# Kernel optimization log

Hardware: AMD Instinct MI355X
Metric: run time of the kernel (lower is better)

Reference implementation:

```python
import jax, jax.numpy as jnp
import numpy as np

NUM_CLASSES = 1000
N, C = 8192, 256

def setup_inputs() -> dict:
    key = jax.random.key(0)
    k1, k2, k3 = jax.random.split(key, 3)
    p = jax.random.normal(k1, (N, C), dtype=jnp.float32)
    z = jax.random.normal(k2, (N, C), dtype=jnp.float32)
    t = jax.random.uniform(k3, (N, NUM_CLASSES), dtype=jnp.float32, minval=1e-4, maxval=1.0)
    targets = t / jnp.sum(t, axis=1, keepdims=True)  # valid soft-label distribution
    return {"p": p, "z": z, "targets": targets}

def reference(p, z, targets):
    z = jax.lax.stop_gradient(z)  # z.detach()
    # F.normalize(dim=1), eps=1e-12
    p = p / jnp.maximum(jnp.linalg.norm(p, axis=1, keepdims=True), 1e-12)
    zn = z / jnp.maximum(jnp.linalg.norm(z, axis=1, keepdims=True), 1e-12)
    dot_product = -jnp.matmul(p, zn.T)  # [N, N]
    # entropy of soft targets, NaN rows (any exact-zero entry) zeroed
    prod = targets * jnp.log(targets)
    entr = -jnp.sum(prod, axis=1)
    entr = jnp.where(jnp.isnan(entr), 0.0, entr)
    norm_entr = entr / jnp.log(jnp.float32(NUM_CLASSES))
    r = 1.0 - norm_entr
    mask1 = jnp.outer(r, r)  # [N, N]
    # cosine similarity Gram of targets (torch cosine_similarity eps=1e-8)
    tnorm = jnp.linalg.norm(targets, axis=1)
    denom = jnp.maximum(tnorm[:, None] * tnorm[None, :], 1e-8)
    mask2 = jnp.matmul(targets, targets.T) / denom  # [N, N]
    n = dot_product.shape[0]
    mask_anchor_out = 1.0 - jnp.eye(n, dtype=dot_product.dtype)
    mask_combined = mask1 * mask2 * mask_anchor_out
    sel = dot_product * mask_combined
    # mean over nonzero entries (jit-safe: sum / count of nonzeros)
    nz = (sel != 0.0)
    return jnp.sum(sel) / jnp.sum(nz).astype(sel.dtype)
```

## Files before the change

### kernel.cpp

```cpp
#include <hip/hip_runtime.h>
#include <math.h>

#define NROWS 8192
#define CDIM 256
#define KDIM 1000
#define KPAD 1024

#define BC 128
#define BK 64
#define BI 8

typedef __attribute__((ext_vector_type(8))) short bf16x8;
typedef __attribute__((ext_vector_type(4))) float f32x4;
typedef _Float16 f16;
typedef __attribute__((ext_vector_type(4))) _Float16 f16x4;

__device__ __forceinline__ unsigned short f2bf(float x) {
  unsigned int u = __float_as_uint(x);
  u += 0x7fffu + ((u >> 16) & 1u);
  return (unsigned short)(u >> 16);
}
__device__ __forceinline__ float bf2f(unsigned short h) {
  return __uint_as_float(((unsigned int)h) << 16);
}

__device__ __forceinline__ void gl16(const void* g, void* l) {
  __builtin_amdgcn_global_load_lds(
      (const __attribute__((address_space(1))) unsigned int*)g,
      (__attribute__((address_space(3))) unsigned int*)l, 16, 0, 0);
}

__global__ __launch_bounds__(256, 4) void prep_kernel(
    const float* __restrict__ p, const float* __restrict__ z,
    const float* __restrict__ t,
    unsigned short* __restrict__ gAhi, unsigned short* __restrict__ gAlo,
    unsigned short* __restrict__ gBhi, unsigned short* __restrict__ gBlo,
    unsigned short* __restrict__ gUhi, unsigned short* __restrict__ gUlo,
    float* __restrict__ diag) {
  __shared__ float tbuf[8 * 1028];
  __shared__ float st_s[8], uu_s[8], sa_s[8], sb_s[8];
  __shared__ double r_s[8];
  const int tid = threadIdx.x;
  const int w = tid >> 6, lane = tid & 63;
  const int stripe = blockIdx.x;
  const int istep = stripe >> 2;
  const int qtr = stripe & 3;
  const int i0 = stripe * 8;

#pragma unroll
  for (int rr = 0; rr < 2; ++rr) {
    const int row = 2 * w + rr;
    const float* trow = t + (size_t)(i0 + row) * KDIM;
    float stt = 0.f, ent = 0.f, zfl = 0.f;
#pragma unroll
    for (int c = 0; c < 4; ++c) {
      const int k4 = c * 64 + lane;
      float4 v = make_float4(0.f, 0.f, 0.f, 0.f);
      if (k4 < 250) {
        v = *(const float4*)(trow + k4 * 4);
        const float vv[4] = {v.x, v.y, v.z, v.w};
#pragma unroll
        for (int q = 0; q < 4; ++q) {
          stt += vv[q] * vv[q];
          if (vv[q] > 0.f) ent += vv[q] * logf(vv[q]);
          else zfl = 1.f;
        }
      }
      *(float4*)&tbuf[row * 1028 + k4 * 4] = v;
    }
#pragma unroll
    for (int off = 32; off; off >>= 1) {
      stt += __shfl_xor(stt, off);
      ent += __shfl_xor(ent, off);
      zfl += __shfl_xor(zfl, off);
    }
    if (lane == 0) {
      const float tnorm = sqrtf(stt);
      st_s[row] = 1.f / tnorm;
      uu_s[row] = stt / (tnorm * tnorm);
      const float entr = (zfl > 0.f) ? 0.f : (-ent);
      r_s[row] = 1.0 - (double)entr / log(1000.0);
    }
  }
  __syncthreads();

#pragma unroll
  for (int it = 0; it < 4; ++it) {
    const int item = it * 256 + tid;
    const int kt = item >> 7;
    const int kf = (item >> 4) & 7;
    const int cl = item & 15;
    const int kcl = kf * 16 + cl;
    unsigned int hi[4], lo[4];
#pragma unroll
    for (int q = 0; q < 4; ++q) {
      const int r0 = 2 * q, r1 = r0 + 1;
      const float v0 = tbuf[r0 * 1028 + kt * 128 + kcl] * st_s[r0];
      const float v1 = tbuf[r1 * 1028 + kt * 128 + kcl] * st_s[r1];
      const unsigned short h0 = f2bf(v0), h1 = f2bf(v1);
      hi[q] = (unsigned int)h0 | ((unsigned int)h1 << 16);
      const unsigned short e0 = f2bf(v0 - bf2f(h0));
      const unsigned short e1 = f2bf(v1 - bf2f(h1));
      lo[q] = (unsigned int)e0 | ((unsigned int)e1 << 16);
    }
    const size_t off = ((size_t)(kt * 256 + istep)) * 8192
                       + (size_t)kf * 1024 + (size_t)(qtr * 16 + cl) * 16;
    *(uint4*)((char*)gUhi + off) = make_uint4(hi[0], hi[1], hi[2], hi[3]);
    *(uint4*)((char*)gUlo + off) = make_uint4(lo[0], lo[1], lo[2], lo[3]);
  }
  __syncthreads();

  float* ptile = tbuf;
  float* ztile = tbuf + 8 * 260;
#pragma unroll
  for (int rr = 0; rr < 2; ++rr) {
    const int row = 2 * w + rr;
    const float* prow = p + (size_t)(i0 + row) * CDIM;
    const float* zrow = z + (size_t)(i0 + row) * CDIM;
    const float4 pv = *(const float4*)(prow + lane * 4);
    const float4 zv = *(const float4*)(zrow + lane * 4);
    *(float4*)&ptile[row * 260 + lane * 4] = pv;
    *(float4*)&ztile[row * 260 + lane * 4] = zv;
    float sp = pv.x * pv.x + pv.y * pv.y + pv.z * pv.z + pv.w * pv.w;
    float sz = zv.x * zv.x + zv.y * zv.y + zv.z * zv.z + zv.w * zv.w;
    float spz = pv.x * zv.x + pv.y * zv.y + pv.z * zv.z + pv.w * zv.w;
#pragma unroll
    for (int off = 32; off; off >>= 1) {
      sp += __shfl_xor(sp, off);
      sz += __shfl_xor(sz, off);
      spz += __shfl_xor(spz, off);
    }
    if (lane == 0) {
      const double r = r_s[row];
      const float pnorm = sqrtf(sp), znorm = sqrtf(sz);
      const float sav = (float)(r / fmax((double)pnorm, 1e-12));
      const float sbv = (float)(r / fmax((double)znorm, 1e-12));
      sa_s[row] = sav; sb_s[row] = sbv;
      diag[i0 + row] = spz * sav * sbv * uu_s[row];
    }
  }
  __syncthreads();

  {
    const int cfg = tid >> 4;
    const int cl = tid & 15;
    const int crd = cfg * 16 + cl;
#pragma unroll 1
    for (int which = 0; which < 2; ++which) {
      const float* tile = which ? ztile : ptile;
      const float* ss = which ? sb_s : sa_s;
      unsigned short* ghi = which ? gBhi : gAhi;
      unsigned short* glo = which ? gBlo : gAlo;
      unsigned int hi[4], lo[4];
#pragma unroll
      for (int q = 0; q < 4; ++q) {
        const int r0 = 2 * q, r1 = r0 + 1;
        const float v0 = tile[r0 * 260 + crd] * ss[r0];
        const float v1 = tile[r1 * 260 + crd] * ss[r1];
        const unsigned short h0 = f2bf(v0), h1 = f2bf(v1);
        hi[q] = (unsigned int)h0 | ((unsigned int)h1 << 16);
        const unsigned short e0 = f2bf(v0 - bf2f(h0));
        const unsigned short e1 = f2bf(v1 - bf2f(h1));
        lo[q] = (unsigned int)e0 | ((unsigned int)e1 << 16);
      }
      const size_t off = ((size_t)((cfg >> 3) * 256 + istep)) * 8192
                         + (size_t)(cfg & 7) * 1024 + (size_t)(qtr * 16 + cl) * 16;
      *(uint4*)((char*)ghi + off) = make_uint4(hi[0], hi[1], hi[2], hi[3]);
      *(uint4*)((char*)glo + off) = make_uint4(lo[0], lo[1], lo[2], lo[3]);
    }
  }
}

__global__ __launch_bounds__(512, 2) void mfma_gemm_kernel(
    const unsigned short* __restrict__ gAhi, const unsigned short* __restrict__ gAlo,
    const unsigned short* __restrict__ gBhi, const unsigned short* __restrict__ gBlo,
    const unsigned short* __restrict__ gUhi, const unsigned short* __restrict__ gUlo,
    f16* __restrict__ part1, f16* __restrict__ part2, int steps) {
  __shared__ unsigned short lds[3][6][4096];
  const int tid = threadIdx.x;
  const int lane = tid & 63;
  const int wid = tid >> 6;
  const int wr = wid >> 1, wc = wid & 1;
  const int ct = blockIdx.x, kt = blockIdx.y, zc = blockIdx.z;
  const int istep0 = zc * steps;

  f32x4 acc1[2][4], acc2[2][4];
#pragma unroll
  for (int c = 0; c < 2; ++c)
#pragma unroll
    for (int k = 0; k < 4; ++k) {
      acc1[c][k] = (f32x4){0.f, 0.f, 0.f, 0.f};
      acc2[c][k] = (f32x4){0.f, 0.f, 0.f, 0.f};
    }

  const char* sA0 = (const char*)gAhi;
  const char* sA1 = (const char*)gAlo;
  const char* sB0 = (const char*)gBhi;
  const char* sB1 = (const char*)gBlo;
  const char* sU0 = (const char*)gUhi;
  const char* sU1 = (const char*)gUlo;

  auto stage = [&](int buf, int s) {
    const size_t ab = ((size_t)(ct * 256 + istep0 + s)) * 8192 + (size_t)tid * 16;
    const size_t ub = ((size_t)(kt * 256 + istep0 + s)) * 8192 + (size_t)tid * 16;
    gl16(sA0 + ab, &lds[buf][0][tid * 8]);
    gl16(sA1 + ab, &lds[buf][1][tid * 8]);
    gl16(sB0 + ab, &lds[buf][2][tid * 8]);
    gl16(sB1 + ab, &lds[buf][3][tid * 8]);
    gl16(sU0 + ub, &lds[buf][4][tid * 8]);
    gl16(sU1 + ub, &lds[buf][5][tid * 8]);
  };

  stage(0, 0);
  if (steps > 1) stage(1, 1);
  for (int s = 0; s < steps; ++s) {
    const int cur = s % 3;
    if (s < steps - 1) {
      asm volatile("s_waitcnt vmcnt(6)" ::: "memory");
    } else {
      asm volatile("s_waitcnt vmcnt(0)" ::: "memory");
    }
    __builtin_amdgcn_s_barrier();
    asm volatile("" ::: "memory");
    if (s + 2 < steps) stage((s + 2) % 3, s + 2);

    bf16x8 ah[2], al[2], bh[2], bl[2], uh[4], ul[4];
#pragma unroll
    for (int c = 0; c < 2; ++c) {
      const int cf = wr * 2 + c;
      ah[c] = *(const bf16x8*)&lds[cur][0][(cf * 64 + lane) * 8];
      al[c] = *(const bf16x8*)&lds[cur][1][(cf * 64 + lane) * 8];
      bh[c] = *(const bf16x8*)&lds[cur][2][(cf * 64 + lane) * 8];
      bl[c] = *(const bf16x8*)&lds[cur][3][(cf * 64 + lane) * 8];
    }
#pragma unroll
    for (int k = 0; k < 4; ++k) {
      const int kf = wc * 4 + k;
      uh[k] = *(const bf16x8*)&lds[cur][4][(kf * 64 + lane) * 8];
      ul[k] = *(const bf16x8*)&lds[cur][5][(kf * 64 + lane) * 8];
    }
    __builtin_amdgcn_s_setprio(1);
#pragma unroll
    for (int k = 0; k < 4; ++k)
#pragma unroll
      for (int c = 0; c < 2; ++c) {
        acc1[c][k] = __builtin_amdgcn_mfma_f32_16x16x32_bf16(ah[c], uh[k], acc1[c][k], 0, 0, 0);
        acc1[c][k] = __builtin_amdgcn_mfma_f32_16x16x32_bf16(al[c], uh[k], acc1[c][k], 0, 0, 0);
        acc1[c][k] = __builtin_amdgcn_mfma_f32_16x16x32_bf16(ah[c], ul[k], acc1[c][k], 0, 0, 0);
        acc2[c][k] = __builtin_amdgcn_mfma_f32_16x16x32_bf16(bh[c], uh[k], acc2[c][k], 0, 0, 0);
        acc2[c][k] = __builtin_amdgcn_mfma_f32_16x16x32_bf16(bl[c], uh[k], acc2[c][k], 0, 0, 0);
        acc2[c][k] = __builtin_amdgcn_mfma_f32_16x16x32_bf16(bh[c], ul[k], acc2[c][k], 0, 0, 0);
      }
    __builtin_amdgcn_s_setprio(0);
  }

  f16* o1 = part1 + (size_t)zc * (CDIM * KPAD);
  f16* o2 = part2 + (size_t)zc * (CDIM * KPAD);
#pragma unroll
  for (int c = 0; c < 2; ++c)
#pragma unroll
    for (int k = 0; k < 4; ++k)
#pragma unroll
      for (int j = 0; j < 4; ++j) {
        const int cg = ct * 128 + (wr * 2 + c) * 16 + (lane >> 4) * 4 + j;
        const int kg = kt * 128 + (wc * 4 + k) * 16 + (lane & 15);
        o1[(size_t)cg * KPAD + kg] = (f16)acc1[c][k][j];
        o2[(size_t)cg * KPAD + kg] = (f16)acc2[c][k][j];
      }
}

__global__ __launch_bounds__(256) void reduce_h_kernel(
    const f16* __restrict__ part1, const f16* __restrict__ part2,
    double* __restrict__ bsum, int split) {
  const int tid = threadIdx.x;
  const size_t base = ((size_t)blockIdx.x * 256 + tid) * 4;
  double m1[4] = {0, 0, 0, 0}, m2[4] = {0, 0, 0, 0};
#pragma unroll 4
  for (int zz = 0; zz < split; ++zz) {
    const f16x4 a = *(const f16x4*)(part1 + (size_t)zz * (CDIM * KPAD) + base);
    const f16x4 b = *(const f16x4*)(part2 + (size_t)zz * (CDIM * KPAD) + base);
#pragma unroll
    for (int e = 0; e < 4; ++e) {
      m1[e] += (double)(float)a[e];
      m2[e] += (double)(float)b[e];
    }
  }
  double s = 0.0;
#pragma unroll
  for (int e = 0; e < 4; ++e) s += m1[e] * m2[e];
  __shared__ double red[256];
  red[tid] = s;
  __syncthreads();
  for (int off = 128; off; off >>= 1) {
    if (tid < off) red[tid] += red[tid + off];
    __syncthreads();
  }
  if (tid == 0) bsum[blockIdx.x] = red[0];
}

__global__ __launch_bounds__(256) void rowstats_kernel(
    const float* __restrict__ p, const float* __restrict__ z,
    const float* __restrict__ t,
    float* __restrict__ sa, float* __restrict__ sb,
    float* __restrict__ st, float* __restrict__ diag) {
  const int i = blockIdx.x;
  const int tid = threadIdx.x;
  const float pv = p[(size_t)i * CDIM + tid];
  const float zv = z[(size_t)i * CDIM + tid];
  float sp = pv * pv, sz = zv * zv, spz = pv * zv;
  float stt = 0.f, ent = 0.f, zfl = 0.f;
  const float* trow = t + (size_t)i * KDIM;
  for (int k = tid; k < KDIM; k += 256) {
    const float tv = trow[k];
    stt += tv * tv;
    if (tv > 0.f) ent += tv * logf(tv);
    else zfl = 1.f;
  }
#pragma unroll
  for (int off = 32; off; off >>= 1) {
    sp  += __shfl_down(sp, off);
    sz  += __shfl_down(sz, off);
    spz += __shfl_down(spz, off);
    stt += __shfl_down(stt, off);
    ent += __shfl_down(ent, off);
    zfl += __shfl_down(zfl, off);
  }
  __shared__ float wred[4][6];
  const int wid = tid >> 6, lane = tid & 63;
  if (lane == 0) {
    wred[wid][0] = sp;  wred[wid][1] = sz;  wred[wid][2] = spz;
    wred[wid][3] = stt; wred[wid][4] = ent; wred[wid][5] = zfl;
  }
  __syncthreads();
  if (tid == 0) {
    sp  = wred[0][0] + wred[1][0] + wred[2][0] + wred[3][0];
    sz  = wred[0][1] + wred[1][1] + wred[2][1] + wred[3][1];
    spz = wred[0][2] + wred[1][2] + wred[2][2] + wred[3][2];
    stt = wred[0][3] + wred[1][3] + wred[2][3] + wred[3][3];
    ent = wred[0][4] + wred[1][4] + wred[2][4] + wred[3][4];
    zfl = wred[0][5] + wred[1][5] + wred[2][5] + wred[3][5];
    const float pnorm = sqrtf(sp);
    const float znorm = sqrtf(sz);
    const float tnorm = sqrtf(stt);
    const float entr = (zfl > 0.f) ? 0.f : (-ent);
    const double r = 1.0 - (double)entr / log(1000.0);
    const float sav = (float)(r / fmax((double)pnorm, 1e-12));
    const float sbv = (float)(r / fmax((double)znorm, 1e-12));
    const float stv = 1.f / tnorm;
    const float uu = stt / (tnorm * tnorm);
    sa[i] = sav; sb[i] = sbv; st[i] = stv;
    diag[i] = spz * sav * sbv * uu;
  }
}

__global__ __launch_bounds__(256) void fp32_gemm_kernel(
    const float* __restrict__ p, const float* __restrict__ z,
    const float* __restrict__ t,
    const float* __restrict__ sa, const float* __restrict__ sb,
    const float* __restrict__ st,
    float* __restrict__ part1, float* __restrict__ part2, int ichunk) {
  __shared__ float As[BI][BC];
  __shared__ float Bs[BI][BC];
  __shared__ float Us[BI][BK];
  const int tid = threadIdx.x;
  const int c0 = blockIdx.x * BC;
  const int k0 = blockIdx.y * BK;
  const int i0 = blockIdx.z * ichunk;
  float acc1[8][4] = {{0.f}};
  float acc2[8][4] = {{0.f}};
  const int tc = tid & 15;
  const int tk = tid >> 4;
  const int lrow = tid >> 5;
  const int lcolA = (tid & 31) * 4;
  const int lcolU = (tid & 31) * 2;
  for (int ib = 0; ib < ichunk; ib += BI) {
    const int i = i0 + ib + lrow;
    const float sav = sa[i], sbv = sb[i], stv = st[i];
    const float4 pv = *(const float4*)(p + (size_t)i * CDIM + c0 + lcolA);
    const float4 zv = *(const float4*)(z + (size_t)i * CDIM + c0 + lcolA);
    const int kk = k0 + lcolU;
    const float u0 = (kk     < KDIM) ? t[(size_t)i * KDIM + kk]     * stv : 0.f;
    const float u1 = (kk + 1 < KDIM) ? t[(size_t)i * KDIM + kk + 1] * stv : 0.f;
    __syncthreads();
    *(float4*)&As[lrow][lcolA] = make_float4(pv.x * sav, pv.y * sav, pv.z * sav, pv.w * sav);
    *(float4*)&Bs[lrow][lcolA] = make_float4(zv.x * sbv, zv.y * sbv, zv.z * sbv, zv.w * sbv);
    Us[lrow][lcolU] = u0;
    Us[lrow][lcolU + 1] = u1;
    __syncthreads();
#pragma unroll
    for (int ii = 0; ii < BI; ++ii) {
      const float4 a0 = *(const float4*)&As[ii][tc * 8];
      const float4 a1 = *(const float4*)&As[ii][tc * 8 + 4];
      const float4 b0 = *(const float4*)&Bs[ii][tc * 8];
      const float4 b1 = *(const float4*)&Bs[ii][tc * 8 + 4];
      const float4 u  = *(const float4*)&Us[ii][tk * 4];
      const float a[8] = {a0.x, a0.y, a0.z, a0.w, a1.x, a1.y, a1.z, a1.w};
      const float b[8] = {b0.x, b0.y, b0.z, b0.w, b1.x, b1.y, b1.z, b1.w};
      const float uv[4] = {u.x, u.y, u.z, u.w};
#pragma unroll
      for (int m = 0; m < 8; ++m)
#pragma unroll
        for (int n = 0; n < 4; ++n) {
          acc1[m][n] = fmaf(a[m], uv[n], acc1[m][n]);
          acc2[m][n] = fmaf(b[m], uv[n], acc2[m][n]);
        }
    }
  }
  float* o1 = part1 + (size_t)blockIdx.z * (CDIM * KPAD);
  float* o2 = part2 + (size_t)blockIdx.z * (CDIM * KPAD);
#pragma unroll
  for (int m = 0; m < 8; ++m) {
    const int c = c0 + tc * 8 + m;
    const int k = k0 + tk * 4;
    *(float4*)&o1[(size_t)c * KPAD + k] = *(const float4*)acc1[m];
    *(float4*)&o2[(size_t)c * KPAD + k] = *(const float4*)acc2[m];
  }
}

__global__ __launch_bounds__(256) void reduce_kernel(
    const float* __restrict__ part1, const float* __restrict__ part2,
    double* __restrict__ bsum, int split) {
  const int tid = threadIdx.x;
  double s = 0.0;
  for (int r = 0; r < 4; ++r) {
    const size_t idx = (size_t)blockIdx.x * 1024 + (size_t)r * 256 + tid;
    double m1 = 0.0, m2 = 0.0;
    for (int zz = 0; zz < split; ++zz) {
      m1 += (double)part1[(size_t)zz * (CDIM * KPAD) + idx];
      m2 += (double)part2[(size_t)zz * (CDIM * KPAD) + idx];
    }
    s += m1 * m2;
  }
  __shared__ double red[256];
  red[tid] = s;
  __syncthreads();
  for (int off = 128; off; off >>= 1) {
    if (tid < off) red[tid] += red[tid + off];
    __syncthreads();
  }
  if (tid == 0) bsum[blockIdx.x] = red[0];
}

__global__ __launch_bounds__(256) void final_kernel(
    const double* __restrict__ bsum, const float* __restrict__ diag,
    float* __restrict__ out, int nb) {
  const int tid = threadIdx.x;
  double s = 0.0;
  for (int i = tid; i < nb; i += 256) s += bsum[i];
  double d = 0.0;
  for (int i = tid; i < NROWS; i += 256) d += (double)diag[i];
  __shared__ double red[256];
  red[tid] = s;
  __syncthreads();
  for (int off = 128; off; off >>= 1) {
    if (tid < off) red[tid] += red[tid + off];
    __syncthreads();
  }
  double s_all = red[0];
  __syncthreads();
  red[tid] = d;
  __syncthreads();
  for (int off = 128; off; off >>= 1) {
    if (tid < off) red[tid] += red[tid + off];
    __syncthreads();
  }
  if (tid == 0) {
    const double s_diag = red[0];
    const double sel_sum = -(s_all - s_diag);
    const double cnt = (double)NROWS * (double)NROWS - (double)NROWS;
    out[0] = (float)(sel_sum / cnt);
  }
}

extern "C" void kernel_launch(void* const* d_in, const int* in_sizes, int n_in,
                              void* d_out, int out_size, void* d_ws, size_t ws_size,
                              hipStream_t stream) {
  const float* p = (const float*)d_in[0];
  const float* z = (const float*)d_in[1];
  const float* t = (const float*)d_in[2];
  float* out = (float*)d_out;
  char* ws = (char*)d_ws;

  float* sa = (float*)ws;
  float* sb = sa + NROWS;
  float* st = sb + NROWS;
  float* diag = st + NROWS;
  const size_t statsB = (size_t)4 * NROWS * sizeof(float);

  const size_t planeA = (size_t)2 * 256 * 8 * 1024;
  const size_t planeU = (size_t)8 * 256 * 8 * 1024;
  const size_t chunkH = (size_t)CDIM * KPAD * 2;
  const size_t chunkF = (size_t)CDIM * KPAD * 4;

  int split = 16;
  while (split > 4 &&
         statsB + 4 * planeA + 2 * planeU + (size_t)split * 2 * chunkH + 8192 > ws_size)
    split >>= 1;
  const bool use_mfma =
      statsB + 4 * planeA + 2 * planeU + (size_t)split * 2 * chunkH + 8192 <= ws_size;

  if (use_mfma) {
    char* base = ws + statsB;
    unsigned short* gAhi = (unsigned short*)(base);
    unsigned short* gAlo = (unsigned short*)(base + planeA);
    unsigned short* gBhi = (unsigned short*)(base + 2 * planeA);
    unsigned short* gBlo = (unsigned short*)(base + 3 * planeA);
    unsigned short* gUhi = (unsigned short*)(base + 4 * planeA);
    unsigned short* gUlo = (unsigned short*)(base + 4 * planeA + planeU);
    f16* part1 = (f16*)(base + 4 * planeA + 2 * planeU);
    f16* part2 = part1 + (size_t)split * (CDIM * KPAD);
    double* bsum = (double*)(part2 + (size_t)split * (CDIM * KPAD));
    const int steps = (NROWS / split) / 32;

    hipLaunchKernelGGL(prep_kernel, dim3(1024), dim3(256), 0, stream,
                       p, z, t, gAhi, gAlo, gBhi, gBlo, gUhi, gUlo, diag);
    hipLaunchKernelGGL(mfma_gemm_kernel, dim3(2, 8, split), dim3(512), 0, stream,
                       gAhi, gAlo, gBhi, gBlo, gUhi, gUlo, part1, part2, steps);
    hipLaunchKernelGGL(reduce_h_kernel, dim3(256), dim3(256), 0, stream,
                       part1, part2, bsum, split);
    hipLaunchKernelGGL(final_kernel, dim3(1), dim3(256), 0, stream,
                       bsum, diag, out, 256);
  } else {
    int osplit = 16;
    while (osplit > 1 &&
           statsB + (size_t)osplit * chunkF * 2 + 8192 > ws_size)
      osplit >>= 1;
    float* part1 = (float*)(ws + statsB);
    float* part2 = part1 + (size_t)osplit * (CDIM * KPAD);
    double* bsum = (double*)(part2 + (size_t)osplit * (CDIM * KPAD));
    hipLaunchKernelGGL(rowstats_kernel, dim3(NROWS), dim3(256), 0, stream,
                       p, z, t, sa, sb, st, diag);
    hipLaunchKernelGGL(fp32_gemm_kernel, dim3(CDIM / BC, KPAD / BK, osplit),
                       dim3(256), 0, stream,
                       p, z, t, sa, sb, st, part1, part2, NROWS / osplit);
    hipLaunchKernelGGL(reduce_kernel, dim3(256), dim3(256), 0, stream,
                       part1, part2, bsum, osplit);
    hipLaunchKernelGGL(final_kernel, dim3(1), dim3(256), 0, stream,
                       bsum, diag, out, 256);
  }
}
```

Measured before the change: 65.34 us.

## Halve GEMM block to 4 waves with larger per-wave C tile

Shrinks the MFMA GEMM block from 512 to 256 threads. Each wave now covers 4 C-fragments instead of 2, so each U fragment loaded from LDS feeds more MFMAs, and U is loaded in two halves to limit register pressure. Each thread issues twice as many global-to-LDS copies per stage, with the vmcnt wait adjusted to match. This cuts LDS read traffic per MFMA but raises VGPR use (64 accumulators) and halves the waves per block, which may reduce latency hiding.

```diff
diff --git a/kernel.cpp b/kernel.cpp
--- a/kernel.cpp
+++ b/kernel.cpp
@@ -171,7 +171,7 @@
   }
 }
 
-__global__ __launch_bounds__(512, 2) void mfma_gemm_kernel(
+__global__ __launch_bounds__(256, 1) void mfma_gemm_kernel(
     const unsigned short* __restrict__ gAhi, const unsigned short* __restrict__ gAlo,
     const unsigned short* __restrict__ gBhi, const unsigned short* __restrict__ gBlo,
     const unsigned short* __restrict__ gUhi, const unsigned short* __restrict__ gUlo,
@@ -184,31 +184,32 @@
   const int ct = blockIdx.x, kt = blockIdx.y, zc = blockIdx.z;
   const int istep0 = zc * steps;
 
-  f32x4 acc1[2][4], acc2[2][4];
-#pragma unroll
-  for (int c = 0; c < 2; ++c)
+  f32x4 acc1[4][4], acc2[4][4];
+#pragma unroll
+  for (int c = 0; c < 4; ++c)
 #pragma unroll
     for (int k = 0; k < 4; ++k) {
       acc1[c][k] = (f32x4){0.f, 0.f, 0.f, 0.f};
       acc2[c][k] = (f32x4){0.f, 0.f, 0.f, 0.f};
     }
 
-  const char* sA0 = (const char*)gAhi;
-  const char* sA1 = (const char*)gAlo;
-  const char* sB0 = (const char*)gBhi;
-  const char* sB1 = (const char*)gBlo;
-  const char* sU0 = (const char*)gUhi;
-  const char* sU1 = (const char*)gUlo;
+  const char* sP[6] = {(const char*)gAhi, (const char*)gAlo,
+                       (const char*)gBhi, (const char*)gBlo,
+                       (const char*)gUhi, (const char*)gUlo};
 
   auto stage = [&](int buf, int s) {
     const size_t ab = ((size_t)(ct * 256 + istep0 + s)) * 8192 + (size_t)tid * 16;
     const size_t ub = ((size_t)(kt * 256 + istep0 + s)) * 8192 + (size_t)tid * 16;
-    gl16(sA0 + ab, &lds[buf][0][tid * 8]);
-    gl16(sA1 + ab, &lds[buf][1][tid * 8]);
-    gl16(sB0 + ab, &lds[buf][2][tid * 8]);
-    gl16(sB1 + ab, &lds[buf][3][tid * 8]);
-    gl16(sU0 + ub, &lds[buf][4][tid * 8]);
-    gl16(sU1 + ub, &lds[buf][5][tid * 8]);
+#pragma unroll
+    for (int pl = 0; pl < 4; ++pl) {
+      gl16(sP[pl] + ab, &lds[buf][pl][tid * 8]);
+      gl16(sP[pl] + ab + 4096, &lds[buf][pl][(tid + 256) * 8]);
+    }
+#pragma unroll
+    for (int pl = 4; pl < 6; ++pl) {
+      gl16(sP[pl] + ub, &lds[buf][pl][tid * 8]);
+      gl16(sP[pl] + ub + 4096, &lds[buf][pl][(tid + 256) * 8]);
+    }
   };
 
   stage(0, 0);
@@ -216,7 +217,7 @@
   for (int s = 0; s < steps; ++s) {
     const int cur = s % 3;
     if (s < steps - 1) {
-      asm volatile("s_waitcnt vmcnt(6)" ::: "memory");
+      asm volatile("s_waitcnt vmcnt(12)" ::: "memory");
     } else {
       asm volatile("s_waitcnt vmcnt(0)" ::: "memory");
     }
@@ -224,45 +225,51 @@
     asm volatile("" ::: "memory");
     if (s + 2 < steps) stage((s + 2) % 3, s + 2);
 
-    bf16x8 ah[2], al[2], bh[2], bl[2], uh[4], ul[4];
-#pragma unroll
-    for (int c = 0; c < 2; ++c) {
-      const int cf = wr * 2 + c;
+    bf16x8 ah[4], al[4], bh[4], bl[4];
+#pragma unroll
+    for (int c = 0; c < 4; ++c) {
+      const int cf = wr * 4 + c;
       ah[c] = *(const bf16x8*)&lds[cur][0][(cf * 64 + lane) * 8];
       al[c] = *(const bf16x8*)&lds[cur][1][(cf * 64 + lane) * 8];
       bh[c] = *(const bf16x8*)&lds[cur][2][(cf * 64 + lane) * 8];
       bl[c] = *(const bf16x8*)&lds[cur][3][(cf * 64 + lane) * 8];
     }
-#pragma unroll
-    for (int k = 0; k < 4; ++k) {
-      const int kf = wc * 4 + k;
-      uh[k] = *(const bf16x8*)&lds[cur][4][(kf * 64 + lane) * 8];
-      ul[k] = *(const bf16x8*)&lds[cur][5][(kf * 64 + lane) * 8];
-    }
     __builtin_amdgcn_s_setprio(1);
 #pragma unroll
-    for (int k = 0; k < 4; ++k)
-#pragma unroll
-      for (int c = 0; c < 2; ++c) {
-        acc1[c][k] = __builtin_amdgcn_mfma_f32_16x16x32_bf16(ah[c], uh[k], acc1[c][k], 0, 0, 0);
-        acc1[c][k] = __builtin_amdgcn_mfma_f32_16x16x32_bf16(al[c], uh[k], acc1[c][k], 0, 0, 0);
-        acc1[c][k] = __builtin_amdgcn_mfma_f32_16x16x32_bf16(ah[c], ul[k], acc1[c][k], 0, 0, 0);
-        acc2[c][k] = __builtin_amdgcn_mfma_f32_16x16x32_bf16(bh[c], uh[k], acc2[c][k], 0, 0, 0);
-        acc2[c][k] = __builtin_amdgcn_mfma_f32_16x16x32_bf16(bl[c], uh[k], acc2[c][k], 0, 0, 0);
-        acc2[c][k] = __builtin_amdgcn_mfma_f32_16x16x32_bf16(bh[c], ul[k], acc2[c][k], 0, 0, 0);
+    for (int kh = 0; kh < 2; ++kh) {
+      bf16x8 uh[2], ul[2];
+#pragma unroll
+      for (int k2 = 0; k2 < 2; ++k2) {
+        const int kf = wc * 4 + kh * 2 + k2;
+        uh[k2] = *(const bf16x8*)&lds[cur][4][(kf * 64 + lane) * 8];
+        ul[k2] = *(const bf16x8*)&lds[cur][5][(kf * 64 + lane) * 8];
       }
+#pragma unroll
+      for (int k2 = 0; k2 < 2; ++k2) {
+        const int k = kh * 2 + k2;
+#pragma unroll
+        for (int c = 0; c < 4; ++c) {
+          acc1[c][k] = __builtin_amdgcn_mfma_f32_16x16x32_bf16(ah[c], uh[k2], acc1[c][k], 0, 0, 0);
+          acc1[c][k] = __builtin_amdgcn_mfma_f32_16x16x32_bf16(al[c], uh[k2], acc1[c][k], 0, 0, 0);
+          acc1[c][k] = __builtin_amdgcn_mfma_f32_16x16x32_bf16(ah[c], ul[k2], acc1[c][k], 0, 0, 0);
+          acc2[c][k] = __builtin_amdgcn_mfma_f32_16x16x32_bf16(bh[c], uh[k2], acc2[c][k], 0, 0, 0);
+          acc2[c][k] = __builtin_amdgcn_mfma_f32_16x16x32_bf16(bl[c], uh[k2], acc2[c][k], 0, 0, 0);
+          acc2[c][k] = __builtin_amdgcn_mfma_f32_16x16x32_bf16(bh[c], ul[k2], acc2[c][k], 0, 0, 0);
+        }
+      }
+    }
     __builtin_amdgcn_s_setprio(0);
   }
 
   f16* o1 = part1 + (size_t)zc * (CDIM * KPAD);
   f16* o2 = part2 + (size_t)zc * (CDIM * KPAD);
 #pragma unroll
-  for (int c = 0; c < 2; ++c)
+  for (int c = 0; c < 4; ++c)
 #pragma unroll
     for (int k = 0; k < 4; ++k)
 #pragma unroll
       for (int j = 0; j < 4; ++j) {
-        const int cg = ct * 128 + (wr * 2 + c) * 16 + (lane >> 4) * 4 + j;
+        const int cg = ct * 128 + (wr * 4 + c) * 16 + (lane >> 4) * 4 + j;
         const int kg = kt * 128 + (wc * 4 + k) * 16 + (lane & 15);
         o1[(size_t)cg * KPAD + kg] = (f16)acc1[c][k][j];
         o2[(size_t)cg * KPAD + kg] = (f16)acc2[c][k][j];
@@ -514,7 +521,7 @@
 
     hipLaunchKernelGGL(prep_kernel, dim3(1024), dim3(256), 0, stream,
                        p, z, t, gAhi, gAlo, gBhi, gBlo, gUhi, gUlo, diag);
-    hipLaunchKernelGGL(mfma_gemm_kernel, dim3(2, 8, split), dim3(512), 0, stream,
+    hipLaunchKernelGGL(mfma_gemm_kernel, dim3(2, 8, split), dim3(256), 0, stream,
                        gAhi, gAlo, gBhi, gBlo, gUhi, gUlo, part1, part2, steps);
     hipLaunchKernelGGL(reduce_h_kernel, dim3(256), dim3(256), 0, stream,
                        part1, part2, bsum, split);
```

New measurement: 65.62 us. No clear change (+0.4%).
